# Optimization experiments

Hardware: AMD Instinct MI355X
Metric: run time of the kernel (lower is better)

The kernel has to match this reference:

```python
import jax, jax.numpy as jnp
import numpy as np

N = 10000
E = 160000
D = 512
EDGE_DIM = 128
L = 3
LN_EPS = 1e-5


def setup_inputs() -> dict:
    key = jax.random.key(0)
    ks = jax.random.split(key, 16)
    s = 0.02
    return {
        "x": jax.random.normal(ks[0], (N, D), dtype=jnp.float32),
        "edge_index": jax.random.randint(ks[1], (2, E), 0, N, dtype=jnp.int64),
        "edge_attr": jax.random.normal(ks[2], (E, EDGE_DIM), dtype=jnp.float32),
        # per-layer GINEConv edge projection Linear(edge_dim -> d_in); here d_in == D for all layers
        "We": jax.random.normal(ks[3], (L, EDGE_DIM, D), dtype=jnp.float32) * s,
        "be": jnp.zeros((L, D), dtype=jnp.float32),
        "eps": jnp.zeros((L,), dtype=jnp.float32),  # train_eps=True, init 0
        # per-layer MLP: Linear(D->D), ReLU, Linear(D->D)
        "W1": jax.random.normal(ks[4], (L, D, D), dtype=jnp.float32) * s,
        "b1": jnp.zeros((L, D), dtype=jnp.float32),
        "W2": jax.random.normal(ks[5], (L, D, D), dtype=jnp.float32) * s,
        "b2": jnp.zeros((L, D), dtype=jnp.float32),
        # per-layer LayerNorm
        "gamma": jnp.ones((L, D), dtype=jnp.float32),
        "beta": jnp.zeros((L, D), dtype=jnp.float32),
        # final Linear(D->D)
        "Wf": jax.random.normal(ks[6], (D, D), dtype=jnp.float32) * s,
        "bf": jnp.zeros((D,), dtype=jnp.float32),
    }


def reference(x, edge_index, edge_attr, We, be, eps, W1, b1, W2, b2, gamma, beta, Wf, bf):
    src = edge_index[0]  # x_j (source)
    dst = edge_index[1]  # aggregation target i
    n = x.shape[0]
    h = x
    for l in range(L):
        # GINEConv message: relu(x_j + lin(edge_attr)), scatter-add at dst
        e = jax.nn.relu(h[src] + edge_attr @ We[l] + be[l])  # [E, D]
        agg = jax.ops.segment_sum(e, dst, num_segments=n)     # [N, D]
        g = (1.0 + eps[l]) * h + agg
        # 2-layer MLP
        g = jax.nn.relu(g @ W1[l] + b1[l]) @ W2[l] + b2[l]
        # ReLU then LayerNorm (dropout p=0)
        g = jax.nn.relu(g)
        mu = jnp.mean(g, axis=-1, keepdims=True)
        var = jnp.mean(jnp.square(g - mu), axis=-1, keepdims=True)
        h = (g - mu) * jax.lax.rsqrt(var + LN_EPS) * gamma[l] + beta[l]
    return h @ Wf + bf
```

## Files before the change

### kernel.cpp

```cpp
#include <hip/hip_runtime.h>

#define NN 10000
#define EE 160000
#define DD 512
#define EDIM 128
#define LLAYERS 3
#define LN_EPS 1e-5f

typedef __attribute__((ext_vector_type(8))) short bf16x8;
typedef __attribute__((ext_vector_type(4))) float f32x4;
typedef __attribute__((ext_vector_type(4))) unsigned int u32x4;

__device__ __forceinline__ unsigned short f2b(float f) {
    union { float f; unsigned u; } v; v.f = f;
    unsigned r = (v.u + 0x7fffu + ((v.u >> 16) & 1u)) >> 16;
    return (unsigned short)r;
}
__device__ __forceinline__ float b2f(unsigned short s) {
    union { unsigned u; float f; } v; v.u = ((unsigned)s) << 16;
    return v.f;
}
__device__ __forceinline__ unsigned short f2h(float f) {
    _Float16 h = (_Float16)f;
    unsigned short u; __builtin_memcpy(&u, &h, 2);
    return u;
}
__device__ __forceinline__ float h2f(unsigned short u) {
    _Float16 h; __builtin_memcpy(&h, &u, 2);
    return (float)h;
}

__global__ __launch_bounds__(256) void hist_kernel(
    const int* __restrict__ dstv, int* __restrict__ deg)
{
    int e = blockIdx.x * 256 + threadIdx.x;
    if (e < EE) atomicAdd(&deg[dstv[e]], 1);
}

__global__ __launch_bounds__(256) void scan_kernel(
    const int* __restrict__ deg, int* __restrict__ base, int* __restrict__ cursor)
{
    __shared__ int sums[256];
    const int t = threadIdx.x;
    const int CH = 40;
    int lo = t * CH;
    int hi = lo + CH; if (hi > NN) hi = NN;
    int s = 0;
    for (int i = lo; i < hi; i++) s += deg[i];
    sums[t] = s;
    __syncthreads();
    for (int off = 1; off < 256; off <<= 1) {
        int v = (t >= off) ? sums[t - off] : 0;
        __syncthreads();
        sums[t] += v;
        __syncthreads();
    }
    int run = (t == 0) ? 0 : sums[t - 1];
    for (int i = lo; i < hi; i++) {
        base[i] = run; cursor[i] = run;
        run += deg[i];
    }
}

__global__ __launch_bounds__(256) void scatter_kernel(
    const int* __restrict__ srcv, const int* __restrict__ dstv,
    int* __restrict__ cursor,
    int* __restrict__ ssrc, int* __restrict__ sdst, int* __restrict__ perm)
{
    int e = blockIdx.x * 256 + threadIdx.x;
    if (e < EE) {
        int d = dstv[e];
        int pos = atomicAdd(&cursor[d], 1);
        ssrc[pos] = srcv[e];
        sdst[pos] = d;
        perm[pos] = e;
    }
}

__global__ __launch_bounds__(256) void transpose_bf16_kernel(
    const float* __restrict__ src, unsigned short* __restrict__ dst, int K, int N)
{
    __shared__ float t[32][33];
    const int x = threadIdx.x & 31;
    const int y = threadIdx.x >> 5;
    const int bn = blockIdx.x * 32;
    const int bk = blockIdx.y * 32;
    #pragma unroll
    for (int j = 0; j < 32; j += 8)
        t[y + j][x] = src[(size_t)(bk + y + j) * N + bn + x];
    __syncthreads();
    #pragma unroll
    for (int j = 0; j < 32; j += 8)
        dst[(size_t)(bn + y + j) * K + bk + x] = f2b(t[x][y + j]);
}

__global__ __launch_bounds__(256) void cvt_bf16_kernel(
    const float* __restrict__ src, unsigned short* __restrict__ dst)
{
    int i = blockIdx.x * 256 + threadIdx.x;
    float4 v = ((const float4*)src)[i];
    uint2 o;
    o.x = (unsigned)f2b(v.x) | ((unsigned)f2b(v.y) << 16);
    o.y = (unsigned)f2b(v.z) | ((unsigned)f2b(v.w) << 16);
    ((uint2*)dst)[i] = o;
}

__global__ __launch_bounds__(256) void gather_cvt_kernel(
    const float* __restrict__ ea, const int* __restrict__ perm,
    unsigned short* __restrict__ out, int elo)
{
    int i = blockIdx.x * 256 + threadIdx.x;
    int r = i >> 5, c4 = (i & 31) * 4;
    const float* p = ea + (size_t)perm[elo + r] * EDIM + c4;
    float4 v = *(const float4*)p;
    uint2 o;
    o.x = (unsigned)f2b(v.x) | ((unsigned)f2b(v.y) << 16);
    o.y = (unsigned)f2b(v.z) | ((unsigned)f2b(v.w) << 16);
    *(uint2*)&out[(size_t)r * EDIM + c4] = o;
}

#define MEP 136
template <int KDIM, bool RELU, int OUT>
__global__ __launch_bounds__(256) void tile_gemm(
    const unsigned short* __restrict__ A,
    const unsigned short* __restrict__ WT,
    const float* __restrict__ bias,
    void* __restrict__ Cout, int M)
{
    __shared__ unsigned short sA[128 * MEP];

    const int tid  = threadIdx.x;
    const int c0   = blockIdx.x * 128;
    const int m0   = blockIdx.y * 128;
    const int w    = tid >> 6;
    const int lane = tid & 63;
    const int quad = lane >> 4;
    const int l16  = lane & 15;
    const int mh   = (w & 1) * 64;
    const int nsl  = (w >> 1) * 64;

    f32x4 acc[4][4];
    #pragma unroll
    for (int mr = 0; mr < 4; mr++)
        #pragma unroll
        for (int nb = 0; nb < 4; nb++)
            acc[mr][nb] = (f32x4){0.f, 0.f, 0.f, 0.f};

    for (int kc = 0; kc < KDIM; kc += 128) {
        if (kc) __syncthreads();
        for (int i = tid; i < 128 * 16; i += 256) {
            int r = i >> 4, seg = i & 15;
            int gm = m0 + r;
            u32x4 v = (u32x4){0u, 0u, 0u, 0u};
            if (gm < M)
                v = *(const u32x4*)&A[(size_t)gm * KDIM + kc + seg * 8];
            *(u32x4*)&sA[r * MEP + seg * 8] = v;
        }
        __syncthreads();
        #pragma unroll
        for (int ks = 0; ks < 4; ks++) {
            const int ko = ks * 32 + quad * 8;
            bf16x8 a[4];
            #pragma unroll
            for (int mr = 0; mr < 4; mr++)
                a[mr] = *(const bf16x8*)&sA[(mh + mr * 16 + l16) * MEP + ko];
            bf16x8 b[4];
            #pragma unroll
            for (int nb = 0; nb < 4; nb++)
                b[nb] = *(const bf16x8*)&WT[(size_t)(c0 + nsl + nb * 16 + l16) * KDIM + kc + ko];
            #pragma unroll
            for (int mr = 0; mr < 4; mr++)
                #pragma unroll
                for (int nb = 0; nb < 4; nb++)
                    acc[mr][nb] = __builtin_amdgcn_mfma_f32_16x16x32_bf16(a[mr], b[nb], acc[mr][nb], 0, 0, 0);
        }
    }

    if (OUT == 2) {
        float* Co = (float*)Cout;
        #pragma unroll
        for (int mr = 0; mr < 4; mr++) {
            const int rb = m0 + mh + mr * 16 + quad * 4;
            #pragma unroll
            for (int nb = 0; nb < 4; nb++) {
                const int c = c0 + nsl + nb * 16 + l16;
                const float bv = bias[c];
                const f32x4 v = acc[mr][nb];
                #pragma unroll
                for (int reg = 0; reg < 4; reg++) {
                    int gm = rb + reg;
                    if (gm < M) {
                        float val = v[reg] + bv;
                        if (RELU) val = fmaxf(val, 0.f);
                        Co[(size_t)gm * DD + c] = val;
                    }
                }
            }
        }
    } else {
        __syncthreads();
        #pragma unroll
        for (int mr = 0; mr < 4; mr++) {
            const int lr = mh + mr * 16 + quad * 4;
            #pragma unroll
            for (int nb = 0; nb < 4; nb++) {
                const int lc = nsl + nb * 16 + l16;
                const float bv = bias[c0 + lc];
                const f32x4 v = acc[mr][nb];
                #pragma unroll
                for (int reg = 0; reg < 4; reg++) {
                    float val = v[reg] + bv;
                    if (RELU) val = fmaxf(val, 0.f);
                    sA[(lr + reg) * MEP + lc] = (OUT == 0) ? f2b(val) : f2h(val);
                }
            }
        }
        __syncthreads();
        unsigned short* Co = (unsigned short*)Cout;
        for (int i = tid; i < 128 * 16; i += 256) {
            int r = i >> 4, seg = i & 15;
            int gm = m0 + r;
            if (gm < M) {
                u32x4 v = *(const u32x4*)&sA[r * MEP + seg * 8];
                if (OUT == 1)
                    __builtin_nontemporal_store(v, (u32x4*)&Co[(size_t)gm * DD + c0 + seg * 8]);
                else
                    *(u32x4*)&Co[(size_t)gm * DD + c0 + seg * 8] = v;
            }
        }
    }
}

__global__ __launch_bounds__(256) void agg_kernel(
    const unsigned short* __restrict__ h_bf,
    const unsigned short* __restrict__ msg,
    const int* __restrict__ ssrc,
    const int* __restrict__ basep,
    const int* __restrict__ degp,
    const float* __restrict__ epsp,
    float* __restrict__ aggp,
    unsigned short* __restrict__ aprime,
    int elo, int ehi, int first, int last)
{
    const int d  = blockIdx.x;
    const int b0 = basep[d];
    const int b1 = b0 + degp[d];
    int lo = b0 > elo ? b0 : elo;
    int hi = b1 < ehi ? b1 : ehi;
    if (!first && !last && lo >= hi) return;

    const int t  = threadIdx.x;
    const int c2 = t * 2;

    float a0 = 0.f, a1 = 0.f;
    if (!first) {
        float2 pv = *(const float2*)&aggp[(size_t)d * DD + c2];
        a0 = pv.x; a1 = pv.y;
    }
    int p = lo;
    for (; p + 4 <= hi; p += 4) {
        const int s0 = ssrc[p],     s1 = ssrc[p + 1];
        const int s2 = ssrc[p + 2], s3 = ssrc[p + 3];
        unsigned m0v = __builtin_nontemporal_load((const unsigned*)&msg[(size_t)(p     - elo) * DD + c2]);
        unsigned m1v = __builtin_nontemporal_load((const unsigned*)&msg[(size_t)(p + 1 - elo) * DD + c2]);
        unsigned m2v = __builtin_nontemporal_load((const unsigned*)&msg[(size_t)(p + 2 - elo) * DD + c2]);
        unsigned m3v = __builtin_nontemporal_load((const unsigned*)&msg[(size_t)(p + 3 - elo) * DD + c2]);
        unsigned h0v = *(const unsigned*)&h_bf[(size_t)s0 * DD + c2];
        unsigned h1v = *(const unsigned*)&h_bf[(size_t)s1 * DD + c2];
        unsigned h2v = *(const unsigned*)&h_bf[(size_t)s2 * DD + c2];
        unsigned h3v = *(const unsigned*)&h_bf[(size_t)s3 * DD + c2];
        a0 += fmaxf(h2f((unsigned short)(m0v & 0xffffu)) + b2f((unsigned short)(h0v & 0xffffu)), 0.f);
        a1 += fmaxf(h2f((unsigned short)(m0v >> 16))     + b2f((unsigned short)(h0v >> 16)),     0.f);
        a0 += fmaxf(h2f((unsigned short)(m1v & 0xffffu)) + b2f((unsigned short)(h1v & 0xffffu)), 0.f);
        a1 += fmaxf(h2f((unsigned short)(m1v >> 16))     + b2f((unsigned short)(h1v >> 16)),     0.f);
        a0 += fmaxf(h2f((unsigned short)(m2v & 0xffffu)) + b2f((unsigned short)(h2v & 0xffffu)), 0.f);
        a1 += fmaxf(h2f((unsigned short)(m2v >> 16))     + b2f((unsigned short)(h2v >> 16)),     0.f);
        a0 += fmaxf(h2f((unsigned short)(m3v & 0xffffu)) + b2f((unsigned short)(h3v & 0xffffu)), 0.f);
        a1 += fmaxf(h2f((unsigned short)(m3v >> 16))     + b2f((unsigned short)(h3v >> 16)),     0.f);
    }
    for (; p < hi; p++) {
        const int s = ssrc[p];
        unsigned mv = __builtin_nontemporal_load((const unsigned*)&msg[(size_t)(p - elo) * DD + c2]);
        unsigned hv = *(const unsigned*)&h_bf[(size_t)s * DD + c2];
        a0 += fmaxf(h2f((unsigned short)(mv & 0xffffu)) + b2f((unsigned short)(hv & 0xffffu)), 0.f);
        a1 += fmaxf(h2f((unsigned short)(mv >> 16))     + b2f((unsigned short)(hv >> 16)),     0.f);
    }
    if (last) {
        const float es = 1.0f + epsp[0];
        unsigned hv = *(const unsigned*)&h_bf[(size_t)d * DD + c2];
        unsigned o = (unsigned)f2b(es * b2f((unsigned short)(hv & 0xffffu)) + a0)
                   | ((unsigned)f2b(es * b2f((unsigned short)(hv >> 16))    + a1) << 16);
        *(unsigned*)&aprime[(size_t)d * DD + c2] = o;
    } else {
        *(float2*)&aggp[(size_t)d * DD + c2] = make_float2(a0, a1);
    }
}

__global__ __launch_bounds__(256) void relu_ln_kernel(
    const unsigned short* __restrict__ g2,
    const float* __restrict__ gamma,
    const float* __restrict__ beta,
    unsigned short* __restrict__ hout)
{
    __shared__ float ss[4], ssq[4];
    const int row = blockIdx.x;
    const int tid = threadIdx.x;
    const unsigned short* gr = g2 + (size_t)row * DD;

    float v0 = fmaxf(b2f(gr[tid]), 0.f);
    float v1 = fmaxf(b2f(gr[tid + 256]), 0.f);
    float s  = v0 + v1;
    float sq = v0 * v0 + v1 * v1;
    #pragma unroll
    for (int off = 32; off > 0; off >>= 1) {
        s  += __shfl_down(s, off);
        sq += __shfl_down(sq, off);
    }
    const int wave = tid >> 6;
    const int lane = tid & 63;
    if (lane == 0) { ss[wave] = s; ssq[wave] = sq; }
    __syncthreads();
    if (tid == 0) {
        float S  = ss[0] + ss[1] + ss[2] + ss[3];
        float SQ = ssq[0] + ssq[1] + ssq[2] + ssq[3];
        float mu = S * (1.f / 512.f);
        float var = SQ * (1.f / 512.f) - mu * mu;
        ss[0]  = mu;
        ssq[0] = rsqrtf(var + LN_EPS);
    }
    __syncthreads();
    float mu = ss[0], rstd = ssq[0];
    hout[(size_t)row * DD + tid] =
        f2b((v0 - mu) * rstd * gamma[tid] + beta[tid]);
    hout[(size_t)row * DD + tid + 256] =
        f2b((v1 - mu) * rstd * gamma[tid + 256] + beta[tid + 256]);
}

extern "C" void kernel_launch(void* const* d_in, const int* in_sizes, int n_in,
                              void* d_out, int out_size, void* d_ws, size_t ws_size,
                              hipStream_t stream)
{
    (void)in_sizes; (void)n_in; (void)out_size;

    const float* x          = (const float*)d_in[0];
    const int*   edge_index = (const int*)d_in[1];
    const float* edge_attr  = (const float*)d_in[2];
    const float* We         = (const float*)d_in[3];
    const float* be         = (const float*)d_in[4];
    const float* eps        = (const float*)d_in[5];
    const float* W1         = (const float*)d_in[6];
    const float* b1         = (const float*)d_in[7];
    const float* W2         = (const float*)d_in[8];
    const float* b2         = (const float*)d_in[9];
    const float* gamma      = (const float*)d_in[10];
    const float* beta       = (const float*)d_in[11];
    const float* Wf         = (const float*)d_in[12];
    const float* bf         = (const float*)d_in[13];

    unsigned short* h_bf   = (unsigned short*)d_ws;
    unsigned short* aprime = h_bf + (size_t)NN * DD;
    unsigned short* t1     = aprime + (size_t)NN * DD;
    unsigned short* t2     = t1 + (size_t)NN * DD;
    unsigned short* WeT    = t2 + (size_t)NN * DD;
    unsigned short* W1T    = WeT + (size_t)LLAYERS * DD * EDIM;
    unsigned short* W2T    = W1T + (size_t)LLAYERS * DD * DD;
    unsigned short* WfT    = W2T + (size_t)LLAYERS * DD * DD;
    int* deg    = (int*)(WfT + (size_t)DD * DD);
    int* basep  = deg + NN;
    int* cursor = basep + NN;
    int* ssrc   = cursor + NN;
    int* sdst   = ssrc + EE;
    int* perm   = sdst + EE;
    float* aggp = (float*)(perm + EE);
    unsigned short* ea_hf = (unsigned short*)(aggp + (size_t)NN * DD);

    size_t used = (size_t)((unsigned char*)ea_hf - (unsigned char*)d_ws);
    size_t rem  = ws_size > used ? ws_size - used : 0;
    const size_t EA_FULL  = (size_t)EE * EDIM * 2;
    const size_t MSG_FULL = (size_t)EE * DD * 2;
    int ea_full; long long capE;
    if (rem >= EA_FULL + MSG_FULL) {
        ea_full = 1; capE = EE;
    } else if (rem >= EA_FULL + (size_t)32 * 1024 * 1024) {
        ea_full = 1;
        capE = (long long)((rem - EA_FULL) / ((size_t)DD * 2)) & ~127LL;
    } else {
        ea_full = 0;
        capE = (long long)(rem / ((size_t)(EDIM + DD) * 2)) & ~127LL;
        if (capE < 128) capE = 128;
    }
    if (capE > EE) capE = EE;
    unsigned short* msg = ea_hf + (ea_full ? (size_t)EE * EDIM : (size_t)capE * EDIM);

    const int* srcv = edge_index;
    const int* dstv = edge_index + EE;

    hipMemsetAsync(deg, 0, NN * sizeof(int), stream);
    hist_kernel<<<dim3((EE + 255) / 256), 256, 0, stream>>>(dstv, deg);
    scan_kernel<<<dim3(1), 256, 0, stream>>>(deg, basep, cursor);
    scatter_kernel<<<dim3((EE + 255) / 256), 256, 0, stream>>>(
        srcv, dstv, cursor, ssrc, sdst, perm);

    cvt_bf16_kernel<<<dim3(NN * DD / 4 / 256), 256, 0, stream>>>(x, h_bf);
    for (int l = 0; l < LLAYERS; l++) {
        transpose_bf16_kernel<<<dim3(DD / 32, EDIM / 32), 256, 0, stream>>>(
            We + (size_t)l * EDIM * DD, WeT + (size_t)l * DD * EDIM, EDIM, DD);
        transpose_bf16_kernel<<<dim3(DD / 32, DD / 32), 256, 0, stream>>>(
            W1 + (size_t)l * DD * DD, W1T + (size_t)l * DD * DD, DD, DD);
        transpose_bf16_kernel<<<dim3(DD / 32, DD / 32), 256, 0, stream>>>(
            W2 + (size_t)l * DD * DD, W2T + (size_t)l * DD * DD, DD, DD);
    }
    transpose_bf16_kernel<<<dim3(DD / 32, DD / 32), 256, 0, stream>>>(Wf, WfT, DD, DD);

    if (ea_full)
        gather_cvt_kernel<<<dim3(EE / 8), 256, 0, stream>>>(edge_attr, perm, ea_hf, 0);

    dim3 ggrid(DD / 128, (NN + 127) / 128);

    const int nch = (int)((EE + capE - 1) / capE);
    for (int l = 0; l < LLAYERS; l++) {
        for (int c = 0; c < nch; c++) {
            const int elo = (int)((long long)c * capE);
            const int cnt = (EE - elo < capE) ? (EE - elo) : (int)capE;
            if (!ea_full)
                gather_cvt_kernel<<<dim3(cnt / 8), 256, 0, stream>>>(edge_attr, perm, ea_hf, elo);
            const unsigned short* Ab = ea_full ? ea_hf + (size_t)elo * EDIM : ea_hf;
            tile_gemm<EDIM, false, 1><<<dim3(4, cnt / 128), 256, 0, stream>>>(
                Ab, WeT + (size_t)l * DD * EDIM, be + (size_t)l * DD, msg, cnt);
            agg_kernel<<<dim3(NN), 256, 0, stream>>>(
                h_bf, msg, ssrc, basep, deg, eps + l, aggp, aprime,
                elo, elo + cnt, c == 0 ? 1 : 0, c == nch - 1 ? 1 : 0);
        }
        tile_gemm<DD, true, 0><<<ggrid, 256, 0, stream>>>(
            aprime, W1T + (size_t)l * DD * DD, b1 + (size_t)l * DD, t1, NN);
        tile_gemm<DD, false, 0><<<ggrid, 256, 0, stream>>>(
            t1, W2T + (size_t)l * DD * DD, b2 + (size_t)l * DD, t2, NN);
        relu_ln_kernel<<<dim3(NN), 256, 0, stream>>>(
            t2, gamma + (size_t)l * DD, beta + (size_t)l * DD, h_bf);
    }
    tile_gemm<DD, false, 2><<<ggrid, 256, 0, stream>>>(h_bf, WfT, bf, d_out, NN);
}
```

Baseline: 874.3 us.

## Fuse edge GEMM with scatter-add via dst-sorted segmented atomics

Result: slower. 1.112 ms (+27.2%).

```diff
diff --git a/kernel.cpp b/kernel.cpp
--- a/kernel.cpp
+++ b/kernel.cpp
@@ -120,9 +120,110 @@
 }
 
 #define MEP 136
-template <int KDIM, bool RELU, int OUT>
+
+__global__ __launch_bounds__(256) void fused_edge_kernel(
+    const unsigned short* __restrict__ Abf,
+    const unsigned short* __restrict__ WeT,
+    const float* __restrict__ be,
+    const unsigned short* __restrict__ h_bf,
+    const int* __restrict__ ssrc,
+    const int* __restrict__ sdst,
+    float* __restrict__ agg,
+    int elo)
+{
+    __shared__ unsigned short sA[128 * MEP];
+    __shared__ int sS[128], sD[128];
+
+    const int tid   = threadIdx.x;
+    const int c0    = blockIdx.x * 128;
+    const int e0loc = blockIdx.y * 128;
+    const int e0    = elo + e0loc;
+    const int w     = tid >> 6;
+    const int lane  = tid & 63;
+    const int quad  = lane >> 4;
+    const int l16   = lane & 15;
+    const int mh    = (w & 1) * 64;
+    const int nsl   = (w >> 1) * 64;
+
+    for (int i = tid; i < 128 * 16; i += 256) {
+        int r = i >> 4, seg = i & 15;
+        *(u32x4*)&sA[r * MEP + seg * 8] =
+            *(const u32x4*)&Abf[(size_t)(e0loc + r) * EDIM + seg * 8];
+    }
+    if (tid < 128) {
+        sS[tid] = ssrc[e0 + tid];
+        sD[tid] = sdst[e0 + tid];
+    }
+    __syncthreads();
+
+    f32x4 acc[4][4];
+    #pragma unroll
+    for (int mr = 0; mr < 4; mr++)
+        #pragma unroll
+        for (int nb = 0; nb < 4; nb++)
+            acc[mr][nb] = (f32x4){0.f, 0.f, 0.f, 0.f};
+
+    #pragma unroll
+    for (int ks = 0; ks < 4; ks++) {
+        const int ko = ks * 32 + quad * 8;
+        bf16x8 a[4];
+        #pragma unroll
+        for (int mr = 0; mr < 4; mr++)
+            a[mr] = *(const bf16x8*)&sA[(mh + mr * 16 + l16) * MEP + ko];
+        bf16x8 b[4];
+        #pragma unroll
+        for (int nb = 0; nb < 4; nb++)
+            b[nb] = *(const bf16x8*)&WeT[(size_t)(c0 + nsl + nb * 16 + l16) * EDIM + ko];
+        #pragma unroll
+        for (int mr = 0; mr < 4; mr++)
+            #pragma unroll
+            for (int nb = 0; nb < 4; nb++)
+                acc[mr][nb] = __builtin_amdgcn_mfma_f32_16x16x32_bf16(a[mr], b[nb], acc[mr][nb], 0, 0, 0);
+    }
+
+    __syncthreads();
+    #pragma unroll
+    for (int mr = 0; mr < 4; mr++) {
+        const int lr = mh + mr * 16 + quad * 4;
+        #pragma unroll
+        for (int nb = 0; nb < 4; nb++) {
+            const int lc = nsl + nb * 16 + l16;
+            const float bv = be[c0 + lc];
+            const f32x4 v = acc[mr][nb];
+            #pragma unroll
+            for (int reg = 0; reg < 4; reg++)
+                sA[(lr + reg) * MEP + lc] = f2h(v[reg] + bv);
+        }
+    }
+    __syncthreads();
+
+    const int half = tid >> 7;
+    const int c    = tid & 127;
+    const int gc   = c0 + c;
+    const int r0   = half * 64;
+
+    float run = 0.f;
+    int rd = sD[r0];
+    bool boundary = true;
+    #pragma unroll 8
+    for (int r = r0; r < r0 + 64; ++r) {
+        const int d = sD[r];
+        if (d != rd) {
+            if (boundary) atomicAdd(&agg[(size_t)rd * DD + gc], run);
+            else          agg[(size_t)rd * DD + gc] = run;
+            run = 0.f; rd = d; boundary = false;
+        }
+        const int s = sS[r];
+        run += fmaxf(h2f(sA[r * MEP + c]) + b2f(h_bf[(size_t)s * DD + gc]), 0.f);
+    }
+    atomicAdd(&agg[(size_t)rd * DD + gc], run);
+}
+
+template <bool FUSE, bool RELU, int OUT>
 __global__ __launch_bounds__(256) void tile_gemm(
     const unsigned short* __restrict__ A,
+    const float* __restrict__ aggp,
+    const float* __restrict__ epsp,
     const unsigned short* __restrict__ WT,
     const float* __restrict__ bias,
     void* __restrict__ Cout, int M)
@@ -139,6 +240,8 @@
     const int mh   = (w & 1) * 64;
     const int nsl  = (w >> 1) * 64;
 
+    const float es = FUSE ? (1.0f + epsp[0]) : 0.0f;
+
     f32x4 acc[4][4];
     #pragma unroll
     for (int mr = 0; mr < 4; mr++)
@@ -146,14 +249,30 @@
         for (int nb = 0; nb < 4; nb++)
             acc[mr][nb] = (f32x4){0.f, 0.f, 0.f, 0.f};
 
-    for (int kc = 0; kc < KDIM; kc += 128) {
+    for (int kc = 0; kc < DD; kc += 128) {
         if (kc) __syncthreads();
         for (int i = tid; i < 128 * 16; i += 256) {
             int r = i >> 4, seg = i & 15;
             int gm = m0 + r;
             u32x4 v = (u32x4){0u, 0u, 0u, 0u};
-            if (gm < M)
-                v = *(const u32x4*)&A[(size_t)gm * KDIM + kc + seg * 8];
+            if (gm < M) {
+                v = *(const u32x4*)&A[(size_t)gm * DD + kc + seg * 8];
+                if (FUSE) {
+                    const float* ap = aggp + (size_t)gm * DD + kc + seg * 8;
+                    float4 g0 = *(const float4*)ap;
+                    float4 g1 = *(const float4*)(ap + 4);
+                    u32x4 o;
+                    o.x = (unsigned)f2b(es * b2f((unsigned short)(v.x & 0xffff)) + g0.x)
+                        | ((unsigned)f2b(es * b2f((unsigned short)(v.x >> 16)) + g0.y) << 16);
+                    o.y = (unsigned)f2b(es * b2f((unsigned short)(v.y & 0xffff)) + g0.z)
+                        | ((unsigned)f2b(es * b2f((unsigned short)(v.y >> 16)) + g0.w) << 16);
+                    o.z = (unsigned)f2b(es * b2f((unsigned short)(v.z & 0xffff)) + g1.x)
+                        | ((unsigned)f2b(es * b2f((unsigned short)(v.z >> 16)) + g1.y) << 16);
+                    o.w = (unsigned)f2b(es * b2f((unsigned short)(v.w & 0xffff)) + g1.z)
+                        | ((unsigned)f2b(es * b2f((unsigned short)(v.w >> 16)) + g1.w) << 16);
+                    v = o;
+                }
+            }
             *(u32x4*)&sA[r * MEP + seg * 8] = v;
         }
         __syncthreads();
@@ -167,7 +286,7 @@
             bf16x8 b[4];
             #pragma unroll
             for (int nb = 0; nb < 4; nb++)
-                b[nb] = *(const bf16x8*)&WT[(size_t)(c0 + nsl + nb * 16 + l16) * KDIM + kc + ko];
+                b[nb] = *(const bf16x8*)&WT[(size_t)(c0 + nsl + nb * 16 + l16) * DD + kc + ko];
             #pragma unroll
             for (int mr = 0; mr < 4; mr++)
                 #pragma unroll
@@ -183,8 +302,8 @@
             const int rb = m0 + mh + mr * 16 + quad * 4;
             #pragma unroll
             for (int nb = 0; nb < 4; nb++) {
-                const int c = c0 + nsl + nb * 16 + l16;
-                const float bv = bias[c];
+                const int cc = c0 + nsl + nb * 16 + l16;
+                const float bv = bias[cc];
                 const f32x4 v = acc[mr][nb];
                 #pragma unroll
                 for (int reg = 0; reg < 4; reg++) {
@@ -192,7 +311,7 @@
                     if (gm < M) {
                         float val = v[reg] + bv;
                         if (RELU) val = fmaxf(val, 0.f);
-                        Co[(size_t)gm * DD + c] = val;
+                        Co[(size_t)gm * DD + cc] = val;
                     }
                 }
             }
@@ -211,7 +330,7 @@
                 for (int reg = 0; reg < 4; reg++) {
                     float val = v[reg] + bv;
                     if (RELU) val = fmaxf(val, 0.f);
-                    sA[(lr + reg) * MEP + lc] = (OUT == 0) ? f2b(val) : f2h(val);
+                    sA[(lr + reg) * MEP + lc] = f2b(val);
                 }
             }
         }
@@ -222,77 +341,9 @@
             int gm = m0 + r;
             if (gm < M) {
                 u32x4 v = *(const u32x4*)&sA[r * MEP + seg * 8];
-                if (OUT == 1)
-                    __builtin_nontemporal_store(v, (u32x4*)&Co[(size_t)gm * DD + c0 + seg * 8]);
-                else
-                    *(u32x4*)&Co[(size_t)gm * DD + c0 + seg * 8] = v;
+                *(u32x4*)&Co[(size_t)gm * DD + c0 + seg * 8] = v;
             }
         }
-    }
-}
-
-__global__ __launch_bounds__(256) void agg_kernel(
-    const unsigned short* __restrict__ h_bf,
-    const unsigned short* __restrict__ msg,
-    const int* __restrict__ ssrc,
-    const int* __restrict__ basep,
-    const int* __restrict__ degp,
-    const float* __restrict__ epsp,
-    float* __restrict__ aggp,
-    unsigned short* __restrict__ aprime,
-    int elo, int ehi, int first, int last)
-{
-    const int d  = blockIdx.x;
-    const int b0 = basep[d];
-    const int b1 = b0 + degp[d];
-    int lo = b0 > elo ? b0 : elo;
-    int hi = b1 < ehi ? b1 : ehi;
-    if (!first && !last && lo >= hi) return;
-
-    const int t  = threadIdx.x;
-    const int c2 = t * 2;
-
-    float a0 = 0.f, a1 = 0.f;
-    if (!first) {
-        float2 pv = *(const float2*)&aggp[(size_t)d * DD + c2];
-        a0 = pv.x; a1 = pv.y;
-    }
-    int p = lo;
-    for (; p + 4 <= hi; p += 4) {
-        const int s0 = ssrc[p],     s1 = ssrc[p + 1];
-        const int s2 = ssrc[p + 2], s3 = ssrc[p + 3];
-        unsigned m0v = __builtin_nontemporal_load((const unsigned*)&msg[(size_t)(p     - elo) * DD + c2]);
-        unsigned m1v = __builtin_nontemporal_load((const unsigned*)&msg[(size_t)(p + 1 - elo) * DD + c2]);
-        unsigned m2v = __builtin_nontemporal_load((const unsigned*)&msg[(size_t)(p + 2 - elo) * DD + c2]);
-        unsigned m3v = __builtin_nontemporal_load((const unsigned*)&msg[(size_t)(p + 3 - elo) * DD + c2]);
-        unsigned h0v = *(const unsigned*)&h_bf[(size_t)s0 * DD + c2];
-        unsigned h1v = *(const unsigned*)&h_bf[(size_t)s1 * DD + c2];
-        unsigned h2v = *(const unsigned*)&h_bf[(size_t)s2 * DD + c2];
-        unsigned h3v = *(const unsigned*)&h_bf[(size_t)s3 * DD + c2];
-        a0 += fmaxf(h2f((unsigned short)(m0v & 0xffffu)) + b2f((unsigned short)(h0v & 0xffffu)), 0.f);
-        a1 += fmaxf(h2f((unsigned short)(m0v >> 16))     + b2f((unsigned short)(h0v >> 16)),     0.f);
-        a0 += fmaxf(h2f((unsigned short)(m1v & 0xffffu)) + b2f((unsigned short)(h1v & 0xffffu)), 0.f);
-        a1 += fmaxf(h2f((unsigned short)(m1v >> 16))     + b2f((unsigned short)(h1v >> 16)),     0.f);
-        a0 += fmaxf(h2f((unsigned short)(m2v & 0xffffu)) + b2f((unsigned short)(h2v & 0xffffu)), 0.f);
-        a1 += fmaxf(h2f((unsigned short)(m2v >> 16))     + b2f((unsigned short)(h2v >> 16)),     0.f);
-        a0 += fmaxf(h2f((unsigned short)(m3v & 0xffffu)) + b2f((unsigned short)(h3v & 0xffffu)), 0.f);
-        a1 += fmaxf(h2f((unsigned short)(m3v >> 16))     + b2f((unsigned short)(h3v >> 16)),     0.f);
-    }
-    for (; p < hi; p++) {
-        const int s = ssrc[p];
-        unsigned mv = __builtin_nontemporal_load((const unsigned*)&msg[(size_t)(p - elo) * DD + c2]);
-        unsigned hv = *(const unsigned*)&h_bf[(size_t)s * DD + c2];
-        a0 += fmaxf(h2f((unsigned short)(mv & 0xffffu)) + b2f((unsigned short)(hv & 0xffffu)), 0.f);
-        a1 += fmaxf(h2f((unsigned short)(mv >> 16))     + b2f((unsigned short)(hv >> 16)),     0.f);
-    }
-    if (last) {
-        const float es = 1.0f + epsp[0];
-        unsigned hv = *(const unsigned*)&h_bf[(size_t)d * DD + c2];
-        unsigned o = (unsigned)f2b(es * b2f((unsigned short)(hv & 0xffffu)) + a0)
-                   | ((unsigned)f2b(es * b2f((unsigned short)(hv >> 16))    + a1) << 16);
-        *(unsigned*)&aprime[(size_t)d * DD + c2] = o;
-    } else {
-        *(float2*)&aggp[(size_t)d * DD + c2] = make_float2(a0, a1);
     }
 }
 
@@ -357,14 +408,13 @@
     const float* Wf         = (const float*)d_in[12];
     const float* bf         = (const float*)d_in[13];
 
-    unsigned short* h_bf   = (unsigned short*)d_ws;
-    unsigned short* aprime = h_bf + (size_t)NN * DD;
-    unsigned short* t1     = aprime + (size_t)NN * DD;
-    unsigned short* t2     = t1 + (size_t)NN * DD;
-    unsigned short* WeT    = t2 + (size_t)NN * DD;
-    unsigned short* W1T    = WeT + (size_t)LLAYERS * DD * EDIM;
-    unsigned short* W2T    = W1T + (size_t)LLAYERS * DD * DD;
-    unsigned short* WfT    = W2T + (size_t)LLAYERS * DD * DD;
+    unsigned short* h_bf = (unsigned short*)d_ws;
+    unsigned short* t1   = h_bf + (size_t)NN * DD;
+    unsigned short* t2   = t1 + (size_t)NN * DD;
+    unsigned short* WeT  = t2 + (size_t)NN * DD;
+    unsigned short* W1T  = WeT + (size_t)LLAYERS * DD * EDIM;
+    unsigned short* W2T  = W1T + (size_t)LLAYERS * DD * DD;
+    unsigned short* WfT  = W2T + (size_t)LLAYERS * DD * DD;
     int* deg    = (int*)(WfT + (size_t)DD * DD);
     int* basep  = deg + NN;
     int* cursor = basep + NN;
@@ -376,21 +426,10 @@
 
     size_t used = (size_t)((unsigned char*)ea_hf - (unsigned char*)d_ws);
     size_t rem  = ws_size > used ? ws_size - used : 0;
-    const size_t EA_FULL  = (size_t)EE * EDIM * 2;
-    const size_t MSG_FULL = (size_t)EE * DD * 2;
-    int ea_full; long long capE;
-    if (rem >= EA_FULL + MSG_FULL) {
-        ea_full = 1; capE = EE;
-    } else if (rem >= EA_FULL + (size_t)32 * 1024 * 1024) {
-        ea_full = 1;
-        capE = (long long)((rem - EA_FULL) / ((size_t)DD * 2)) & ~127LL;
-    } else {
-        ea_full = 0;
-        capE = (long long)(rem / ((size_t)(EDIM + DD) * 2)) & ~127LL;
-        if (capE < 128) capE = 128;
-    }
+    long long capE = (long long)(rem / ((size_t)EDIM * 2)) & ~127LL;
+    if (capE < 128) capE = 128;
     if (capE > EE) capE = EE;
-    unsigned short* msg = ea_hf + (ea_full ? (size_t)EE * EDIM : (size_t)capE * EDIM);
+    const int ea_full = (capE == EE);
 
     const int* srcv = edge_index;
     const int* dstv = edge_index + EE;
@@ -419,24 +458,24 @@
 
     const int nch = (int)((EE + capE - 1) / capE);
     for (int l = 0; l < LLAYERS; l++) {
+        hipMemsetAsync(aggp, 0, (size_t)NN * DD * sizeof(float), stream);
         for (int c = 0; c < nch; c++) {
             const int elo = (int)((long long)c * capE);
             const int cnt = (EE - elo < capE) ? (EE - elo) : (int)capE;
             if (!ea_full)
                 gather_cvt_kernel<<<dim3(cnt / 8), 256, 0, stream>>>(edge_attr, perm, ea_hf, elo);
             const unsigned short* Ab = ea_full ? ea_hf + (size_t)elo * EDIM : ea_hf;
-            tile_gemm<EDIM, false, 1><<<dim3(4, cnt / 128), 256, 0, stream>>>(
-                Ab, WeT + (size_t)l * DD * EDIM, be + (size_t)l * DD, msg, cnt);
-            agg_kernel<<<dim3(NN), 256, 0, stream>>>(
-                h_bf, msg, ssrc, basep, deg, eps + l, aggp, aprime,
-                elo, elo + cnt, c == 0 ? 1 : 0, c == nch - 1 ? 1 : 0);
-        }
-        tile_gemm<DD, true, 0><<<ggrid, 256, 0, stream>>>(
-            aprime, W1T + (size_t)l * DD * DD, b1 + (size_t)l * DD, t1, NN);
-        tile_gemm<DD, false, 0><<<ggrid, 256, 0, stream>>>(
-            t1, W2T + (size_t)l * DD * DD, b2 + (size_t)l * DD, t2, NN);
+            fused_edge_kernel<<<dim3(4, cnt / 128), 256, 0, stream>>>(
+                Ab, WeT + (size_t)l * DD * EDIM, be + (size_t)l * DD,
+                h_bf, ssrc, sdst, aggp, elo);
+        }
+        tile_gemm<true, true, 0><<<ggrid, 256, 0, stream>>>(
+            h_bf, aggp, eps + l, W1T + (size_t)l * DD * DD, b1 + (size_t)l * DD, t1, NN);
+        tile_gemm<false, false, 0><<<ggrid, 256, 0, stream>>>(
+            t1, nullptr, nullptr, W2T + (size_t)l * DD * DD, b2 + (size_t)l * DD, t2, NN);
         relu_ln_kernel<<<dim3(NN), 256, 0, stream>>>(
             t2, gamma + (size_t)l * DD, beta + (size_t)l * DD, h_bf);
     }
-    tile_gemm<DD, false, 2><<<ggrid, 256, 0, stream>>>(h_bf, WfT, bf, d_out, NN);
-}
+    tile_gemm<false, false, 2><<<ggrid, 256, 0, stream>>>(
+        h_bf, nullptr, nullptr, WfT, bf, d_out, NN);
+}
```
